# Kernel optimization log

Measured on AMD Instinct MI355X. Metric: run time of the kernel, lower is better.

Reference implementation:

```python
import jax, jax.numpy as jnp
import numpy as np

LMAX_IN = 2      # input signal bandwidth
LMAX_OUT = 4     # pointwise product of two lmax=2 signals has bandwidth 4
RES_BETA = 20
RES_ALPHA = 19
C = 32           # num_channels
N = 2048         # batch (samples/nodes)
S_IN = (LMAX_IN + 1) ** 2   # 9
S_OUT = (LMAX_OUT + 1) ** 2  # 25
G = RES_BETA * RES_ALPHA     # 380 grid points

# l-index for each SH coefficient slot (l repeated 2l+1 times)
LIDX_IN = np.repeat(np.arange(LMAX_IN + 1), 2 * np.arange(LMAX_IN + 1) + 1)
LIDX_OUT = np.repeat(np.arange(LMAX_OUT + 1), 2 * np.arange(LMAX_OUT + 1) + 1)


def _grid_and_sh(lmax_in, lmax_out, res_beta, res_alpha):
    """Real orthonormal spherical harmonics on a Gauss-Legendre x uniform grid,
    plus quadrature weights giving exact analysis up to the grid bandwidth."""
    ct, wb = np.polynomial.legendre.leggauss(res_beta)  # cos(beta) nodes / weights
    st = np.sqrt(np.clip(1.0 - ct * ct, 0.0, None))
    alpha = np.linspace(0.0, 2.0 * np.pi, res_alpha, endpoint=False)
    lmax = max(lmax_in, lmax_out)
    # normalized associated Legendre P[l, m, beta]
    P = np.zeros((lmax + 1, lmax + 1, res_beta))
    P[0, 0] = np.full(res_beta, 1.0 / np.sqrt(4.0 * np.pi))
    for m in range(1, lmax + 1):
        P[m, m] = -np.sqrt((2.0 * m + 1.0) / (2.0 * m)) * st * P[m - 1, m - 1]
    for m in range(lmax):
        P[m + 1, m] = np.sqrt(2.0 * m + 3.0) * ct * P[m, m]
    for m in range(lmax + 1):
        for l in range(m + 2, lmax + 1):
            a = np.sqrt((4.0 * l * l - 1.0) / (l * l - m * m))
            b = np.sqrt(((l - 1.0) ** 2 - m * m) / (4.0 * (l - 1.0) ** 2 - 1.0))
            P[l, m] = a * (ct * P[l - 1, m] - b * P[l - 2, m])
    Y = np.zeros((res_beta, res_alpha, (lmax + 1) ** 2))
    idx = 0
    for l in range(lmax + 1):
        for m in range(-l, l + 1):
            if m == 0:
                Y[:, :, idx] = P[l, 0][:, None]
            elif m > 0:
                Y[:, :, idx] = np.sqrt(2.0) * P[l, m][:, None] * np.cos(m * alpha)[None, :]
            else:
                Y[:, :, idx] = np.sqrt(2.0) * P[l, -m][:, None] * np.sin(-m * alpha)[None, :]
            idx += 1
    Y = Y.reshape(res_beta * res_alpha, (lmax + 1) ** 2)
    w = (wb[:, None] * np.full((1, res_alpha), 2.0 * np.pi / res_alpha)).reshape(-1)
    return (Y[:, : (lmax_in + 1) ** 2].astype(np.float32),
            Y[:, : (lmax_out + 1) ** 2].astype(np.float32),
            w.astype(np.float32))


def setup_inputs() -> dict:
    key = jax.random.key(0)
    k1, k2, k3, k4, k5 = jax.random.split(key, 5)
    Yin_np, Yout_np, w_np = _grid_and_sh(LMAX_IN, LMAX_OUT, RES_BETA, RES_ALPHA)
    return {
        "x": jax.random.normal(k1, (N, 3, S_IN), dtype=jnp.float32),
        "y": jax.random.normal(k2, (N, 3, S_IN), dtype=jnp.float32),
        # per-l channel-expansion weights (e3nn Linear from mul=1 to mul=C)
        "Wx": jax.random.normal(k3, (LMAX_IN + 1, C), dtype=jnp.float32) / jnp.sqrt(1.0),
        "Wy": jax.random.normal(k4, (LMAX_IN + 1, C), dtype=jnp.float32) / jnp.sqrt(1.0),
        # per-l output channel-mixing weights (linear_out_z)
        "Wz": jax.random.normal(k5, (LMAX_OUT + 1, C, C), dtype=jnp.float32) / jnp.sqrt(C),
        "Yin": jnp.asarray(Yin_np),    # [G, S_IN]
        "Yout": jnp.asarray(Yout_np),  # [G, S_OUT]
        "wquad": jnp.asarray(w_np),    # [G]
    }


def reference(x, y, Wx, Wy, Wz, Yin, Yout, wquad):
    lin_in = jnp.asarray(LIDX_IN)
    lin_out = jnp.asarray(LIDX_OUT)
    # linear_in: expand each irrep to C channels (block-diagonal per l)
    xc = jnp.einsum('nvs,sc->ncvs', x, Wx[lin_in])  # [N,C,3,S_IN]
    yc = jnp.einsum('nvs,sc->ncvs', y, Wy[lin_in])
    # to-grid synthesis of 3-vector signals: f(g) = sum_s c_s Y_s(g)
    fx = jnp.einsum('ncvs,gs->ncgv', xc, Yin)       # [N,C,G,3]
    fy = jnp.einsum('ncvs,gs->ncgv', yc, Yin)
    # pointwise cross product on the sphere grid
    fz = jnp.cross(fx, fy)                           # [N,C,G,3]
    # from-grid analysis with quadrature weights
    zc = jnp.einsum('ncgv,g,gt->ncvt', fz, wquad, Yout)  # [N,C,3,S_OUT]
    # linear_out_z: mix channels per output irrep l
    out = jnp.einsum('ncvt,tcd->ndvt', zc, Wz[lin_out])  # [N,C,3,S_OUT]
    return out
```

## Files before the change

kernel.cpp:

```cpp
#include <hip/hip_runtime.h>


#define GG 380

__device__ __forceinline__ bool decode2(int pq, int& s, int& sp) {
    int b, off;
    if (pq < 16) {
        if (pq < 4)       { b = 0; off = pq; }
        else if (pq < 8)  { b = 1; off = pq - 4; }
        else              { b = 2; off = pq - 8; }
    } else if (pq < 48) {
        if (pq < 20)      { b = 3; off = pq - 16; }
        else if (pq < 32) { b = 4; off = pq - 20; }
        else              { b = 5; off = pq - 32; }
    } else {
        if (pq < 56)      { b = 6; off = pq - 48; }
        else if (pq < 72) { b = 7; off = pq - 56; }
        else              { b = 8; off = pq - 72; }
    }
    int ls = b / 3, lsp = b % 3, w = 2 * lsp + 1;
    if (off >= (2 * ls + 1) * w) return false;
    s  = ls * ls + off / w;
    sp = lsp * lsp + off % w;
    return true;
}

__global__ __launch_bounds__(256) void precomp(const float* __restrict__ Wx,
                                               const float* __restrict__ Wy,
                                               const float* __restrict__ Wz,
                                               const float* __restrict__ Yin,
                                               const float* __restrict__ Yout,
                                               const float* __restrict__ wq,
                                               float* __restrict__ Tg,
                                               float* __restrict__ Vg) {
    int bid = blockIdx.x;
    if (bid < 625) {
        int W = bid * 4 + (threadIdx.x >> 6);
        int lane = threadIdx.x & 63;
        int t = W / 100, pq = W % 100;
        int s, sp;
        float acc = 0.f;
        if (decode2(pq, s, sp)) {
#pragma unroll
            for (int i = 0; i < 6; ++i) {
                int g = lane + 64 * i;
                if (g < GG)
                    acc = fmaf(wq[g] * Yin[g * 9 + s],
                               Yin[g * 9 + sp] * Yout[g * 25 + t], acc);
            }
        }
#pragma unroll
        for (int m = 32; m; m >>= 1) acc += __shfl_xor(acc, m, 64);
        if (lane == 0) Tg[W] = acc;
    } else {
        int idx = (bid - 625) * 256 + threadIdx.x;
        if (idx < 1440) {
            int lt = idx / 288, r = idx % 288, b = r / 32, d = r % 32;
            int ls = b / 3, lsp = b % 3;
            float acc = 0.f;
            for (int c = 0; c < 32; ++c)
                acc = fmaf(Wx[ls * 32 + c] * Wy[lsp * 32 + c],
                           Wz[lt * 1024 + c * 32 + d], acc);
            Vg[idx] = acc;
        }
    }
}

__global__ __launch_bounds__(256) void gaunt_main(const float* __restrict__ x,
                                                  const float* __restrict__ y,
                                                  const float* __restrict__ Tg,
                                                  const float* __restrict__ Vg,
                                                  float* __restrict__ out) {
    __shared__ __align__(16) float smem[8856];
    float* xs   = smem;
    float* ys   = smem + 108;
    float* Ps   = smem + 216;
    float* Vs   = smem + 816;
    float* Z    = smem + 2256;
    float* Ts   = smem + 4056;
    float* Zout = smem + 4056;

    const int tid = threadIdx.x;
    const int n0 = blockIdx.x * 2;

    if (tid < 54)       xs[tid]      = x[n0 * 27 + tid];
    else if (tid < 108) ys[tid - 54] = y[n0 * 27 + tid - 54];
    for (int i = tid; i < 625; i += 256)
        ((float4*)Ts)[i] = ((const float4*)Tg)[i];
    for (int i = tid; i < 360; i += 256)
        ((float4*)Vs)[i] = ((const float4*)Vg)[i];
    __syncthreads();

    for (int idx = tid; idx < 600; idx += 256) {
        int row = idx / 100, pq = idx % 100;
        float v = 0.f;
        int s, sp;
        if (decode2(pq, s, sp)) {
            int ni = row / 3, vv = row % 3;
            int a = (vv == 0) ? 1 : ((vv == 1) ? 2 : 0);
            int b = (vv == 0) ? 2 : ((vv == 1) ? 0 : 1);
            v = xs[ni * 27 + a * 9 + s] * ys[ni * 27 + b * 9 + sp]
              - xs[ni * 27 + b * 9 + s] * ys[ni * 27 + a * 9 + sp];
        }
        Ps[idx] = v;
    }
    __syncthreads();

#define DOT4(c, accv) { float4 pv = P4[c], tv = T4[c];                      \
        accv = fmaf(pv.x, tv.x, accv); accv = fmaf(pv.y, tv.y, accv);       \
        accv = fmaf(pv.z, tv.z, accv); accv = fmaf(pv.w, tv.w, accv); }
    if (tid < 150) {
        int t = tid / 6, row = tid % 6;
        const float4* P4 = (const float4*)(Ps + row * 100);
        const float4* T4 = (const float4*)(Ts + t * 100);
        float a0 = 0.f, a1 = 0.f, a2 = 0.f, a3 = 0.f, a4 = 0.f,
              a5 = 0.f, a6 = 0.f, a7 = 0.f, a8 = 0.f;
        DOT4(0, a0)
        DOT4(1, a1)
        DOT4(2, a2)  DOT4(3, a2)
        DOT4(4, a3)
        DOT4(5, a4)  DOT4(6, a4)  DOT4(7, a4)
        DOT4(8, a5)  DOT4(9, a5)  DOT4(10, a5) DOT4(11, a5)
        DOT4(12, a6) DOT4(13, a6)
        DOT4(14, a7) DOT4(15, a7) DOT4(16, a7) DOT4(17, a7)
        DOT4(18, a8) DOT4(19, a8) DOT4(20, a8) DOT4(21, a8)
        DOT4(22, a8) DOT4(23, a8) DOT4(24, a8)
        float* zp = Z + row * 300 + t * 12;
        *(float4*)zp       = make_float4(a0, a1, a2, a3);
        *(float4*)(zp + 4) = make_float4(a4, a5, a6, a7);
        zp[8] = a8;
    }
#undef DOT4
    __syncthreads();

    {
        const int d = tid & 31, g = tid >> 5;
        if (g < 6) {
            const int row = g;
            const int zo = (row / 3) * 2400 + d * 75 + (row % 3) * 25;
            const float* zrow = Z + row * 300;
#pragma unroll
            for (int lt = 0; lt < 5; ++lt) {
                const float* vb = Vs + lt * 288 + d;
                const float v0 = vb[0],   v1 = vb[32],  v2 = vb[64],
                            v3 = vb[96],  v4 = vb[128], v5 = vb[160],
                            v6 = vb[192], v7 = vb[224], v8 = vb[256];
                const int t0 = lt * lt, t1 = (lt + 1) * (lt + 1);
#pragma unroll
                for (int t = t0; t < t1; ++t) {
                    const float* zp = zrow + t * 12;
                    float4 za = *(const float4*)zp;
                    float4 zb = *(const float4*)(zp + 4);
                    float acc = zp[8] * v8;
                    acc = fmaf(za.x, v0, acc); acc = fmaf(za.y, v1, acc);
                    acc = fmaf(za.z, v2, acc); acc = fmaf(za.w, v3, acc);
                    acc = fmaf(zb.x, v4, acc); acc = fmaf(zb.y, v5, acc);
                    acc = fmaf(zb.z, v6, acc); acc = fmaf(zb.w, v7, acc);
                    Zout[zo + t] = acc;
                }
            }
        }
    }
    __syncthreads();

    float4* og = (float4*)(out + (size_t)n0 * 2400);
    const float4* zo4 = (const float4*)Zout;
    for (int i = tid; i < 1200; i += 256) og[i] = zo4[i];
}

extern "C" void kernel_launch(void* const* d_in, const int* in_sizes, int n_in,
                              void* d_out, int out_size, void* d_ws, size_t ws_size,
                              hipStream_t stream) {
    const float* x    = (const float*)d_in[0];
    const float* y    = (const float*)d_in[1];
    const float* Wx   = (const float*)d_in[2];
    const float* Wy   = (const float*)d_in[3];
    const float* Wz   = (const float*)d_in[4];
    const float* Yin  = (const float*)d_in[5];
    const float* Yout = (const float*)d_in[6];
    const float* wq   = (const float*)d_in[7];
    float* out = (float*)d_out;

    float* Tg = (float*)d_ws;
    float* Vg = Tg + 2500;

    precomp<<<631, 256, 0, stream>>>(Wx, Wy, Wz, Yin, Yout, wq, Tg, Vg);
    gaunt_main<<<1024, 256, 0, stream>>>(x, y, Tg, Vg, out);
}
```

Baseline: 21.00 us.

## Fuse Gaunt contraction with output channel mixing to drop Z staging pass

The Vg weight table is padded to 292 floats per output degree so its rows are float4-aligned. Each of the 150 threads now applies the channel-mixing weights to its 9 contraction accumulators in registers and writes all 32 channels straight to Zout. This removes the Z shared-memory staging buffer, one __syncthreads, and the separate 6-warp mixing phase. In exchange, shared memory per block grows, and each thread does 32x more mixing work while leaving the other 106 threads idle.

Result: slower. 23.15 us (+10.2%).

```diff
diff --git a/kernel.cpp b/kernel.cpp
--- a/kernel.cpp
+++ b/kernel.cpp
@@ -54,13 +54,16 @@
         if (lane == 0) Tg[W] = acc;
     } else {
         int idx = (bid - 625) * 256 + threadIdx.x;
-        if (idx < 1440) {
-            int lt = idx / 288, r = idx % 288, b = r / 32, d = r % 32;
-            int ls = b / 3, lsp = b % 3;
+        if (idx < 1460) {
+            int lt = idx / 292, r = idx % 292;
             float acc = 0.f;
-            for (int c = 0; c < 32; ++c)
-                acc = fmaf(Wx[ls * 32 + c] * Wy[lsp * 32 + c],
-                           Wz[lt * 1024 + c * 32 + d], acc);
+            if (r < 288) {
+                int b = r / 32, d = r % 32;
+                int ls = b / 3, lsp = b % 3;
+                for (int c = 0; c < 32; ++c)
+                    acc = fmaf(Wx[ls * 32 + c] * Wy[lsp * 32 + c],
+                               Wz[lt * 1024 + c * 32 + d], acc);
+            }
             Vg[idx] = acc;
         }
     }
@@ -71,14 +74,13 @@
                                                   const float* __restrict__ Tg,
                                                   const float* __restrict__ Vg,
                                                   float* __restrict__ out) {
-    __shared__ __align__(16) float smem[8856];
+    __shared__ __align__(16) float smem[9576];
     float* xs   = smem;
     float* ys   = smem + 108;
     float* Ps   = smem + 216;
-    float* Vs   = smem + 816;
-    float* Z    = smem + 2256;
-    float* Ts   = smem + 4056;
-    float* Zout = smem + 4056;
+    float* Ts   = smem + 816;
+    float* Vs   = smem + 3316;
+    float* Zout = smem + 4776;
 
     const int tid = threadIdx.x;
     const int n0 = blockIdx.x * 2;
@@ -87,7 +89,7 @@
     else if (tid < 108) ys[tid - 54] = y[n0 * 27 + tid - 54];
     for (int i = tid; i < 625; i += 256)
         ((float4*)Ts)[i] = ((const float4*)Tg)[i];
-    for (int i = tid; i < 360; i += 256)
+    for (int i = tid; i < 365; i += 256)
         ((float4*)Vs)[i] = ((const float4*)Vg)[i];
     __syncthreads();
 
@@ -110,7 +112,7 @@
         accv = fmaf(pv.x, tv.x, accv); accv = fmaf(pv.y, tv.y, accv);       \
         accv = fmaf(pv.z, tv.z, accv); accv = fmaf(pv.w, tv.w, accv); }
     if (tid < 150) {
-        int t = tid / 6, row = tid % 6;
+        const int t = tid / 6, row = tid % 6;
         const float4* P4 = (const float4*)(Ps + row * 100);
         const float4* T4 = (const float4*)(Ts + t * 100);
         float a0 = 0.f, a1 = 0.f, a2 = 0.f, a3 = 0.f, a4 = 0.f,
@@ -125,42 +127,46 @@
         DOT4(14, a7) DOT4(15, a7) DOT4(16, a7) DOT4(17, a7)
         DOT4(18, a8) DOT4(19, a8) DOT4(20, a8) DOT4(21, a8)
         DOT4(22, a8) DOT4(23, a8) DOT4(24, a8)
-        float* zp = Z + row * 300 + t * 12;
-        *(float4*)zp       = make_float4(a0, a1, a2, a3);
-        *(float4*)(zp + 4) = make_float4(a4, a5, a6, a7);
-        zp[8] = a8;
+
+        const int lt = (t >= 16) ? 4 : (t >= 9) ? 3 : (t >= 4) ? 2
+                     : (t >= 1) ? 1 : 0;
+        const float* vbase = Vs + lt * 292;
+        const int zo = (row / 3) * 2400 + (row % 3) * 25 + t;
+#pragma unroll
+        for (int dq = 0; dq < 8; ++dq) {
+            const float4 w0 = *(const float4*)(vbase +   0 + dq * 4);
+            const float4 w1 = *(const float4*)(vbase +  32 + dq * 4);
+            const float4 w2 = *(const float4*)(vbase +  64 + dq * 4);
+            const float4 w3 = *(const float4*)(vbase +  96 + dq * 4);
+            const float4 w4 = *(const float4*)(vbase + 128 + dq * 4);
+            const float4 w5 = *(const float4*)(vbase + 160 + dq * 4);
+            const float4 w6 = *(const float4*)(vbase + 192 + dq * 4);
+            const float4 w7 = *(const float4*)(vbase + 224 + dq * 4);
+            const float4 w8 = *(const float4*)(vbase + 256 + dq * 4);
+            float o0 = a8 * w8.x, o1 = a8 * w8.y, o2 = a8 * w8.z, o3 = a8 * w8.w;
+            o0 = fmaf(a0, w0.x, o0); o1 = fmaf(a0, w0.y, o1);
+            o2 = fmaf(a0, w0.z, o2); o3 = fmaf(a0, w0.w, o3);
+            o0 = fmaf(a1, w1.x, o0); o1 = fmaf(a1, w1.y, o1);
+            o2 = fmaf(a1, w1.z, o2); o3 = fmaf(a1, w1.w, o3);
+            o0 = fmaf(a2, w2.x, o0); o1 = fmaf(a2, w2.y, o1);
+            o2 = fmaf(a2, w2.z, o2); o3 = fmaf(a2, w2.w, o3);
+            o0 = fmaf(a3, w3.x, o0); o1 = fmaf(a3, w3.y, o1);
+            o2 = fmaf(a3, w3.z, o2); o3 = fmaf(a3, w3.w, o3);
+            o0 = fmaf(a4, w4.x, o0); o1 = fmaf(a4, w4.y, o1);
+            o2 = fmaf(a4, w4.z, o2); o3 = fmaf(a4, w4.w, o3);
+            o0 = fmaf(a5, w5.x, o0); o1 = fmaf(a5, w5.y, o1);
+            o2 = fmaf(a5, w5.z, o2); o3 = fmaf(a5, w5.w, o3);
+            o0 = fmaf(a6, w6.x, o0); o1 = fmaf(a6, w6.y, o1);
+            o2 = fmaf(a6, w6.z, o2); o3 = fmaf(a6, w6.w, o3);
+            o0 = fmaf(a7, w7.x, o0); o1 = fmaf(a7, w7.y, o1);
+            o2 = fmaf(a7, w7.z, o2); o3 = fmaf(a7, w7.w, o3);
+            Zout[zo + (dq * 4 + 0) * 75] = o0;
+            Zout[zo + (dq * 4 + 1) * 75] = o1;
+            Zout[zo + (dq * 4 + 2) * 75] = o2;
+            Zout[zo + (dq * 4 + 3) * 75] = o3;
+        }
     }
 #undef DOT4
-    __syncthreads();
-
-    {
-        const int d = tid & 31, g = tid >> 5;
-        if (g < 6) {
-            const int row = g;
-            const int zo = (row / 3) * 2400 + d * 75 + (row % 3) * 25;
-            const float* zrow = Z + row * 300;
-#pragma unroll
-            for (int lt = 0; lt < 5; ++lt) {
-                const float* vb = Vs + lt * 288 + d;
-                const float v0 = vb[0],   v1 = vb[32],  v2 = vb[64],
-                            v3 = vb[96],  v4 = vb[128], v5 = vb[160],
-                            v6 = vb[192], v7 = vb[224], v8 = vb[256];
-                const int t0 = lt * lt, t1 = (lt + 1) * (lt + 1);
-#pragma unroll
-                for (int t = t0; t < t1; ++t) {
-                    const float* zp = zrow + t * 12;
-                    float4 za = *(const float4*)zp;
-                    float4 zb = *(const float4*)(zp + 4);
-                    float acc = zp[8] * v8;
-                    acc = fmaf(za.x, v0, acc); acc = fmaf(za.y, v1, acc);
-                    acc = fmaf(za.z, v2, acc); acc = fmaf(za.w, v3, acc);
-                    acc = fmaf(zb.x, v4, acc); acc = fmaf(zb.y, v5, acc);
-                    acc = fmaf(zb.z, v6, acc); acc = fmaf(zb.w, v7, acc);
-                    Zout[zo + t] = acc;
-                }
-            }
-        }
-    }
     __syncthreads();
 
     float4* og = (float4*)(out + (size_t)n0 * 2400);
```

## Reblock Gaunt contraction and channel mixing for register reuse

Applied to the files above, without the earlier changes.

The P·T contraction now runs on 50 threads, each computing three rows per t so each T float4 is loaded once and reused. The channel-mixing stage gives each thread four output channels d via float4 loads of V, with V rows padded to 292 floats so each slab stays 16-byte aligned. The goal is fewer LDS loads per FMA. The cost is less parallelism in the first stage (50 threads instead of 150), unequal loop trip counts per lt in the second stage, and more registers per thread.

Result: slower. 25.81 us (+22.9%).

```diff
diff --git a/kernel.cpp b/kernel.cpp
--- a/kernel.cpp
+++ b/kernel.cpp
@@ -54,31 +54,37 @@
         if (lane == 0) Tg[W] = acc;
     } else {
         int idx = (bid - 625) * 256 + threadIdx.x;
-        if (idx < 1440) {
-            int lt = idx / 288, r = idx % 288, b = r / 32, d = r % 32;
-            int ls = b / 3, lsp = b % 3;
+        if (idx < 1460) {
+            int lt = idx / 292, r = idx % 292;
             float acc = 0.f;
-            for (int c = 0; c < 32; ++c)
-                acc = fmaf(Wx[ls * 32 + c] * Wy[lsp * 32 + c],
-                           Wz[lt * 1024 + c * 32 + d], acc);
+            if (r < 288) {
+                int b = r / 32, d = r % 32;
+                int ls = b / 3, lsp = b % 3;
+                for (int c = 0; c < 32; ++c)
+                    acc = fmaf(Wx[ls * 32 + c] * Wy[lsp * 32 + c],
+                               Wz[lt * 1024 + c * 32 + d], acc);
+            }
             Vg[idx] = acc;
         }
     }
 }
+
+__device__ __constant__ const int BOFC[25] =
+    {0,1,2,2,3,4,4,4,5,5,5,5,6,6,7,7,7,7,8,8,8,8,8,8,8};
 
 __global__ __launch_bounds__(256) void gaunt_main(const float* __restrict__ x,
                                                   const float* __restrict__ y,
                                                   const float* __restrict__ Tg,
                                                   const float* __restrict__ Vg,
                                                   float* __restrict__ out) {
-    __shared__ __align__(16) float smem[8856];
+    __shared__ __align__(16) float smem[8876];
     float* xs   = smem;
     float* ys   = smem + 108;
     float* Ps   = smem + 216;
     float* Vs   = smem + 816;
-    float* Z    = smem + 2256;
-    float* Ts   = smem + 4056;
-    float* Zout = smem + 4056;
+    float* Z    = smem + 2276;
+    float* Ts   = smem + 4076;
+    float* Zout = smem + 4076;
 
     const int tid = threadIdx.x;
     const int n0 = blockIdx.x * 2;
@@ -87,7 +93,7 @@
     else if (tid < 108) ys[tid - 54] = y[n0 * 27 + tid - 54];
     for (int i = tid; i < 625; i += 256)
         ((float4*)Ts)[i] = ((const float4*)Tg)[i];
-    for (int i = tid; i < 360; i += 256)
+    for (int i = tid; i < 365; i += 256)
         ((float4*)Vs)[i] = ((const float4*)Vg)[i];
     __syncthreads();
 
@@ -106,59 +112,87 @@
     }
     __syncthreads();
 
-#define DOT4(c, accv) { float4 pv = P4[c], tv = T4[c];                      \
-        accv = fmaf(pv.x, tv.x, accv); accv = fmaf(pv.y, tv.y, accv);       \
-        accv = fmaf(pv.z, tv.z, accv); accv = fmaf(pv.w, tv.w, accv); }
-    if (tid < 150) {
-        int t = tid / 6, row = tid % 6;
-        const float4* P4 = (const float4*)(Ps + row * 100);
+    if (tid < 50) {
+        const int t = tid >> 1, rh = tid & 1;
         const float4* T4 = (const float4*)(Ts + t * 100);
-        float a0 = 0.f, a1 = 0.f, a2 = 0.f, a3 = 0.f, a4 = 0.f,
-              a5 = 0.f, a6 = 0.f, a7 = 0.f, a8 = 0.f;
-        DOT4(0, a0)
-        DOT4(1, a1)
-        DOT4(2, a2)  DOT4(3, a2)
-        DOT4(4, a3)
-        DOT4(5, a4)  DOT4(6, a4)  DOT4(7, a4)
-        DOT4(8, a5)  DOT4(9, a5)  DOT4(10, a5) DOT4(11, a5)
-        DOT4(12, a6) DOT4(13, a6)
-        DOT4(14, a7) DOT4(15, a7) DOT4(16, a7) DOT4(17, a7)
-        DOT4(18, a8) DOT4(19, a8) DOT4(20, a8) DOT4(21, a8)
-        DOT4(22, a8) DOT4(23, a8) DOT4(24, a8)
-        float* zp = Z + row * 300 + t * 12;
-        *(float4*)zp       = make_float4(a0, a1, a2, a3);
-        *(float4*)(zp + 4) = make_float4(a4, a5, a6, a7);
-        zp[8] = a8;
-    }
-#undef DOT4
-    __syncthreads();
-
-    {
-        const int d = tid & 31, g = tid >> 5;
-        if (g < 6) {
-            const int row = g;
-            const int zo = (row / 3) * 2400 + d * 75 + (row % 3) * 25;
-            const float* zrow = Z + row * 300;
-#pragma unroll
-            for (int lt = 0; lt < 5; ++lt) {
-                const float* vb = Vs + lt * 288 + d;
-                const float v0 = vb[0],   v1 = vb[32],  v2 = vb[64],
-                            v3 = vb[96],  v4 = vb[128], v5 = vb[160],
-                            v6 = vb[192], v7 = vb[224], v8 = vb[256];
-                const int t0 = lt * lt, t1 = (lt + 1) * (lt + 1);
-#pragma unroll
-                for (int t = t0; t < t1; ++t) {
-                    const float* zp = zrow + t * 12;
-                    float4 za = *(const float4*)zp;
-                    float4 zb = *(const float4*)(zp + 4);
-                    float acc = zp[8] * v8;
-                    acc = fmaf(za.x, v0, acc); acc = fmaf(za.y, v1, acc);
-                    acc = fmaf(za.z, v2, acc); acc = fmaf(za.w, v3, acc);
-                    acc = fmaf(zb.x, v4, acc); acc = fmaf(zb.y, v5, acc);
-                    acc = fmaf(zb.z, v6, acc); acc = fmaf(zb.w, v7, acc);
-                    Zout[zo + t] = acc;
-                }
-            }
+        const float4* Q0 = (const float4*)(Ps + (3 * rh + 0) * 100);
+        const float4* Q1 = (const float4*)(Ps + (3 * rh + 1) * 100);
+        const float4* Q2 = (const float4*)(Ps + (3 * rh + 2) * 100);
+        float A0[9], A1[9], A2[9];
+#pragma unroll
+        for (int b = 0; b < 9; ++b) { A0[b] = 0.f; A1[b] = 0.f; A2[b] = 0.f; }
+#pragma unroll
+        for (int c = 0; c < 25; ++c) {
+            const int b = BOFC[c];
+            const float4 tv = T4[c];
+            float4 pv;
+            pv = Q0[c];
+            A0[b] = fmaf(pv.x, tv.x, A0[b]); A0[b] = fmaf(pv.y, tv.y, A0[b]);
+            A0[b] = fmaf(pv.z, tv.z, A0[b]); A0[b] = fmaf(pv.w, tv.w, A0[b]);
+            pv = Q1[c];
+            A1[b] = fmaf(pv.x, tv.x, A1[b]); A1[b] = fmaf(pv.y, tv.y, A1[b]);
+            A1[b] = fmaf(pv.z, tv.z, A1[b]); A1[b] = fmaf(pv.w, tv.w, A1[b]);
+            pv = Q2[c];
+            A2[b] = fmaf(pv.x, tv.x, A2[b]); A2[b] = fmaf(pv.y, tv.y, A2[b]);
+            A2[b] = fmaf(pv.z, tv.z, A2[b]); A2[b] = fmaf(pv.w, tv.w, A2[b]);
+        }
+        float* zp;
+        zp = Z + (3 * rh + 0) * 300 + t * 12;
+        *(float4*)zp = make_float4(A0[0], A0[1], A0[2], A0[3]);
+        *(float4*)(zp + 4) = make_float4(A0[4], A0[5], A0[6], A0[7]);
+        zp[8] = A0[8];
+        zp = Z + (3 * rh + 1) * 300 + t * 12;
+        *(float4*)zp = make_float4(A1[0], A1[1], A1[2], A1[3]);
+        *(float4*)(zp + 4) = make_float4(A1[4], A1[5], A1[6], A1[7]);
+        zp[8] = A1[8];
+        zp = Z + (3 * rh + 2) * 300 + t * 12;
+        *(float4*)zp = make_float4(A2[0], A2[1], A2[2], A2[3]);
+        *(float4*)(zp + 4) = make_float4(A2[4], A2[5], A2[6], A2[7]);
+        zp[8] = A2[8];
+    }
+    __syncthreads();
+
+    if (tid < 240) {
+        const int lt = tid / 48, r = tid % 48, row = r >> 3, dq = r & 7;
+        const float* vb = Vs + lt * 292 + dq * 4;
+        const float4 w0 = *(const float4*)(vb +   0);
+        const float4 w1 = *(const float4*)(vb +  32);
+        const float4 w2 = *(const float4*)(vb +  64);
+        const float4 w3 = *(const float4*)(vb +  96);
+        const float4 w4 = *(const float4*)(vb + 128);
+        const float4 w5 = *(const float4*)(vb + 160);
+        const float4 w6 = *(const float4*)(vb + 192);
+        const float4 w7 = *(const float4*)(vb + 224);
+        const float4 w8 = *(const float4*)(vb + 256);
+        const int t1 = (lt + 1) * (lt + 1);
+        const int zo = (row / 3) * 2400 + (row % 3) * 25 + dq * 300;
+        const float* zrow = Z + row * 300;
+        for (int t = lt * lt; t < t1; ++t) {
+            const float* zp = zrow + t * 12;
+            const float4 za = *(const float4*)zp;
+            const float4 zb = *(const float4*)(zp + 4);
+            const float z8 = zp[8];
+            float o0 = z8 * w8.x, o1 = z8 * w8.y, o2 = z8 * w8.z, o3 = z8 * w8.w;
+            o0 = fmaf(za.x, w0.x, o0); o1 = fmaf(za.x, w0.y, o1);
+            o2 = fmaf(za.x, w0.z, o2); o3 = fmaf(za.x, w0.w, o3);
+            o0 = fmaf(za.y, w1.x, o0); o1 = fmaf(za.y, w1.y, o1);
+            o2 = fmaf(za.y, w1.z, o2); o3 = fmaf(za.y, w1.w, o3);
+            o0 = fmaf(za.z, w2.x, o0); o1 = fmaf(za.z, w2.y, o1);
+            o2 = fmaf(za.z, w2.z, o2); o3 = fmaf(za.z, w2.w, o3);
+            o0 = fmaf(za.w, w3.x, o0); o1 = fmaf(za.w, w3.y, o1);
+            o2 = fmaf(za.w, w3.z, o2); o3 = fmaf(za.w, w3.w, o3);
+            o0 = fmaf(zb.x, w4.x, o0); o1 = fmaf(zb.x, w4.y, o1);
+            o2 = fmaf(zb.x, w4.z, o2); o3 = fmaf(zb.x, w4.w, o3);
+            o0 = fmaf(zb.y, w5.x, o0); o1 = fmaf(zb.y, w5.y, o1);
+            o2 = fmaf(zb.y, w5.z, o2); o3 = fmaf(zb.y, w5.w, o3);
+            o0 = fmaf(zb.z, w6.x, o0); o1 = fmaf(zb.z, w6.y, o1);
+            o2 = fmaf(zb.z, w6.z, o2); o3 = fmaf(zb.z, w6.w, o3);
+            o0 = fmaf(zb.w, w7.x, o0); o1 = fmaf(zb.w, w7.y, o1);
+            o2 = fmaf(zb.w, w7.z, o2); o3 = fmaf(zb.w, w7.w, o3);
+            Zout[zo + t      ] = o0;
+            Zout[zo + t +  75] = o1;
+            Zout[zo + t + 150] = o2;
+            Zout[zo + t + 225] = o3;
         }
     }
     __syncthreads();
```
